# Optimization experiments

Measured on AMD Instinct MI355X. Metric: run time of the kernel, lower is better.

The kernel has to match this reference:

```python
import jax, jax.numpy as jnp
import numpy as np

NB, NL, V, VOCAB, D, TOPK = 16, 64, 16384, 32000, 256, 16
NITER, EARLY, RW = 8, 2, 0.8


def setup_inputs():
    key = jax.random.key(0)
    ks = jax.random.split(key, 8)
    probas = jax.random.uniform(ks[0], (NB, NL, V), dtype=jnp.float32) + 1e-6
    h_d = jax.random.normal(ks[1], (NB, NL, D), dtype=jnp.float32)
    lengths = jax.random.randint(ks[2], (NB,), NL // 2, NL + 1)
    mask = (jnp.arange(NL)[None, :] < lengths[:, None]).astype(jnp.int32)  # prefix mask
    batch_vocab = jax.random.randint(ks[3], (V,), 0, VOCAB)
    emb_table = jax.random.normal(ks[4], (VOCAB, D), dtype=jnp.float32) * 0.02
    W1 = jax.random.normal(ks[5], (2 * D, D), dtype=jnp.float32) * 0.006
    b1 = jnp.zeros((D,), dtype=jnp.float32)
    return {"probas": probas, "h_d": h_d, "mask": mask, "batch_vocab": batch_vocab,
            "emb_table": emb_table, "W1": W1, "b1": b1}


def _forward(probas, h_d, mask, batch_vocab, emb_table, W1, b1):
    maskf = mask.astype(probas.dtype)
    MAP = jnp.argmax(probas, axis=-1)                       # [nb,nl]
    topk_vals, topk_idx = jax.lax.top_k(probas, TOPK)       # [nb,nl,K]
    topk_vals = jnp.where(mask[..., None] < 1, 1.0, topk_vals)
    logits = jnp.log(topk_vals)                             # Categorical(probs) == categorical(log p)
    sLens = jnp.sum(mask, axis=1)                           # [nb]
    one_hot = jnp.arange(NL)[None, :] == (sLens - 1)[:, None]  # one_hot_by_mask: last valid pos
    m2d = (mask[:, :, None] * mask[:, None, :]) > 0
    eyeM = jnp.eye(NL, dtype=probas.dtype)
    h_masked = h_d * maskf[..., None]

    def step(carry, k):
        max_score, best, count, stopped = carry
        choice = jax.random.categorical(k, logits)          # [nb,nl]
        samples = jnp.take_along_axis(topk_idx, choice[..., None], axis=-1)[..., 0]
        samples = jnp.where(one_hot, MAP, samples)
        embs = emb_table[batch_vocab[samples]] * maskf[..., None]   # gather+embed, masked
        new_embs = jax.nn.relu(jnp.concatenate([embs, h_masked], axis=-1) @ W1 + b1)
        Kmat = jnp.einsum('bld,bmd->blm', new_embs, new_embs)       # [nb,nl,nl]
        # det of leading lxl submatrix == det with padded rows/cols replaced by identity
        score = jnp.linalg.det(jnp.where(m2d, Kmat, eyeM))          # [nb]
        improved = score > max_score
        any_imp = jnp.any(improved)
        count = jnp.where(any_imp, 0, count + 1)
        upd = improved & (~stopped)
        stopped = stopped | ((~any_imp) & (count >= EARLY))
        max_score = jnp.where(upd, score, max_score)
        best = jnp.where(upd[:, None], samples, best)
        return (max_score, best, count, stopped), None

    init = (jnp.full((NB,), -jnp.inf, probas.dtype), MAP, jnp.int32(0), jnp.bool_(False))
    keys = jax.random.split(jax.random.key(42), NITER)
    (max_score, best, _, _), _ = jax.lax.scan(step, init, keys)

    # diverse_proba: scatter redist_weight at best choice, (1-rw) elsewhere, renormalize
    am = jnp.where(jnp.arange(V)[None, None, :] == best[:, :, None], RW, 1.0 - RW).astype(probas.dtype)
    x = probas * am
    nm = jnp.sum(x, axis=-1, keepdims=True)
    nm = jnp.where(maskf[..., None] == 0, 1e-10, nm)
    return x / nm, max_score


def reference(probas, h_d, mask, batch_vocab, emb_table, W1, b1):
    return _forward(probas, h_d, mask, batch_vocab, emb_table, W1, b1)
```

## Files before the change

kernel.cpp:

```cpp
#include <hip/hip_runtime.h>
#include <math.h>
#include <stdint.h>


#define TINYF 1.17549435082228750797e-38f

#define KMX(r, c) (((r) * 68) + ((c) ^ ((((r) >> 3) & 7) << 2)))

struct Keys16 { uint32_t k[16]; };

__host__ __device__ inline void tf2x32(uint32_t k0, uint32_t k1,
                                       uint32_t x0, uint32_t x1,
                                       uint32_t* o0, uint32_t* o1) {
  uint32_t ks2 = k0 ^ k1 ^ 0x1BD11BDAu;
  uint32_t ks[3] = {k0, k1, ks2};
  uint32_t v0 = x0 + k0, v1 = x1 + k1;
  const int R0[4] = {13, 15, 26, 6};
  const int R1[4] = {17, 29, 16, 24};
#pragma unroll
  for (int g = 0; g < 5; ++g) {
    const int* RR = (g & 1) ? R1 : R0;
#pragma unroll
    for (int r = 0; r < 4; ++r) {
      v0 += v1;
      v1 = (v1 << RR[r]) | (v1 >> (32 - RR[r]));
      v1 ^= v0;
    }
    v0 += ks[(g + 1) % 3];
    v1 += ks[(g + 2) % 3] + (uint32_t)(g + 1);
  }
  *o0 = v0; *o1 = v1;
}

__device__ inline float logf_ref(float x) { return (float)log((double)x); }

__device__ inline unsigned long long u64max(unsigned long long a,
                                            unsigned long long b) {
  return (a > b) ? a : b;
}

__device__ inline float lane_bcast_f32(float v, int slane) {
  return __uint_as_float(
      (unsigned)__builtin_amdgcn_readlane(__float_as_int(v), slane));
}

template <int CTRL, int RMASK>
__device__ inline void dpp_max_step(unsigned& hi, unsigned& lo) {
  unsigned nh = (unsigned)__builtin_amdgcn_update_dpp(
      0, (int)hi, CTRL, RMASK, 0xF, false);
  unsigned nl = (unsigned)__builtin_amdgcn_update_dpp(
      0, (int)lo, CTRL, RMASK, 0xF, false);
  bool take = (nh > hi) || (nh == hi && nl > lo);
  hi = take ? nh : hi;
  lo = take ? nl : lo;
}

__device__ inline void dpp_reduce_max64(unsigned& hi, unsigned& lo) {
  dpp_max_step<0x111, 0xF>(hi, lo);
  dpp_max_step<0x112, 0xF>(hi, lo);
  dpp_max_step<0x114, 0xF>(hi, lo);
  dpp_max_step<0x118, 0xF>(hi, lo);
  dpp_max_step<0x142, 0xA>(hi, lo);
  dpp_max_step<0x143, 0xC>(hi, lo);
}

__global__ __launch_bounds__(256) void k_topk(const float* __restrict__ probas,
                                              const int* __restrict__ mask,
                                              int* __restrict__ topk_idx,
                                              float* __restrict__ logits,
                                              float* __restrict__ S) {
  int row = blockIdx.x;
  int t = threadIdx.x;
  const float* p = probas + (size_t)row * 16384;
  __shared__ unsigned long long lists[256][16];
  __shared__ float swsum[4];
  __shared__ int lcnt;
  unsigned long long* cand = &lists[0][0];

  cand[t] = 0ull;
  cand[t + 256] = 0ull;
  if (t == 0) lcnt = 0;
  __syncthreads();

  const uint32_t TB = 0x3F7E0000u;
  float sum = 0.f;
  const float4* p4 = (const float4*)p;
#pragma unroll 4
  for (int j = 0; j < 16; ++j) {
    float4 x = p4[t + j * 256];
    int v0 = (t + j * 256) * 4;
    uint32_t u0 = __float_as_uint(x.x), u1 = __float_as_uint(x.y);
    uint32_t u2 = __float_as_uint(x.z), u3 = __float_as_uint(x.w);
    sum += x.x; sum += x.y; sum += x.z; sum += x.w;
    uint32_t um = max(max(u0, u1), max(u2, u3));
    if (um >= TB) {
      if (u0 >= TB) { int s = atomicAdd(&lcnt, 1); if (s < 512)
          cand[s] = ((unsigned long long)u0 << 32) | (unsigned)(~(v0 + 0)); }
      if (u1 >= TB) { int s = atomicAdd(&lcnt, 1); if (s < 512)
          cand[s] = ((unsigned long long)u1 << 32) | (unsigned)(~(v0 + 1)); }
      if (u2 >= TB) { int s = atomicAdd(&lcnt, 1); if (s < 512)
          cand[s] = ((unsigned long long)u2 << 32) | (unsigned)(~(v0 + 2)); }
      if (u3 >= TB) { int s = atomicAdd(&lcnt, 1); if (s < 512)
          cand[s] = ((unsigned long long)u3 << 32) | (unsigned)(~(v0 + 3)); }
    }
  }
#pragma unroll
  for (int off = 32; off >= 1; off >>= 1) sum += __shfl_down(sum, off);
  if ((t & 63) == 0) swsum[t >> 6] = sum;
  __syncthreads();
  if (t == 0) S[row] = ((swsum[0] + swsum[1]) + swsum[2]) + swsum[3];

  int n = lcnt;
  if (n >= 16 && n <= 512) {
    if (t < 64) {
      unsigned long long c[8];
#pragma unroll
      for (int k = 0; k < 8; ++k) c[k] = cand[t + 64 * k];
      unsigned long long win = 0ull;
#pragma unroll
      for (int r = 0; r < 16; ++r) {
        unsigned long long m = c[0];
#pragma unroll
        for (int k = 1; k < 8; ++k) m = u64max(m, c[k]);
#pragma unroll
        for (int off = 32; off >= 1; off >>= 1) {
          unsigned long long o = __shfl_xor(m, off);
          m = u64max(m, o);
        }
        if (t == r) win = m;
#pragma unroll
        for (int k = 0; k < 8; ++k) if (c[k] == m) c[k] = 0ull;
      }
      if (t < 16) {
        int idx = (int)(~(unsigned)(win & 0xFFFFFFFFull));
        float val = __uint_as_float((unsigned)(win >> 32));
        topk_idx[row * 16 + t] = idx;
        logits[row * 16 + t] = (mask[row] == 0) ? 0.0f : logf_ref(val);
      }
    }
    return;
  }

  {
    unsigned long long loc[16];
#pragma unroll
    for (int q = 0; q < 16; ++q) loc[q] = 0ull;
    for (int j = 0; j < 64; ++j) {
      int v = t + j * 256;
      float x = p[v];
      unsigned long long key =
          ((unsigned long long)__float_as_uint(x) << 32) | (unsigned)(~v);
      if (key > loc[15]) {
        loc[15] = key;
#pragma unroll
        for (int q = 15; q > 0; --q) {
          if (loc[q] > loc[q - 1]) {
            unsigned long long tmp = loc[q]; loc[q] = loc[q - 1]; loc[q - 1] = tmp;
          }
        }
      }
    }
    __syncthreads();
#pragma unroll
    for (int q = 0; q < 16; ++q) lists[t][q] = loc[q];
    __syncthreads();
    for (int nl = 128; nl >= 1; nl >>= 1) {
      if (t < nl) {
        unsigned long long M[16];
        int ia = 0, ib = 0;
#pragma unroll
        for (int q = 0; q < 16; ++q) {
          unsigned long long av = lists[t][ia];
          unsigned long long bv = lists[t + nl][ib];
          if (av >= bv) { M[q] = av; ia++; } else { M[q] = bv; ib++; }
        }
#pragma unroll
        for (int q = 0; q < 16; ++q) lists[t][q] = M[q];
      }
      __syncthreads();
    }
    if (t < 16) {
      unsigned long long key = lists[0][t];
      int idx = (int)(~(unsigned)(key & 0xFFFFFFFFull));
      float val = __uint_as_float((unsigned)(key >> 32));
      topk_idx[row * 16 + t] = idx;
      logits[row * 16 + t] = (mask[row] == 0) ? 0.0f : logf_ref(val);
    }
  }
}

__global__ __launch_bounds__(256) void k_sample(Keys16 keys,
                                                const int* __restrict__ mask,
                                                const int* __restrict__ topk_idx,
                                                const float* __restrict__ logits,
                                                int* __restrict__ samples,
                                                int* __restrict__ choice) {
  int tid = blockIdx.x * 256 + threadIdx.x;
  int i = tid >> 10;
  int rbl = tid & 1023;
  int b = rbl >> 6;
  int l = rbl & 63;
  uint32_t k0 = keys.k[2 * i], k1 = keys.k[2 * i + 1];
  int sl = 0;
  for (int m = 0; m < 64; ++m) sl += mask[b * 64 + m];
  float bestv = 0.f; int bestk = 0;
#pragma unroll
  for (int k = 0; k < 16; ++k) {
    uint32_t j = (uint32_t)((b * 64 + l) * 16 + k);
    uint32_t y0, y1;
    tf2x32(k0, k1, 0u, j, &y0, &y1);
    uint32_t bits = y0 ^ y1;
    float f = __uint_as_float((bits >> 9) | 0x3f800000u) - 1.0f;
    float u = fmaxf(TINYF, f * 1.0f + TINYF);
    float t1 = logf_ref(u);
    float g = -logf_ref(-t1);
    float sv = g + logits[rbl * 16 + k];
    if (k == 0 || sv > bestv) { bestv = sv; bestk = k; }
  }
  int ce = (l == sl - 1) ? 0 : bestk;
  choice[tid] = ce;
  samples[tid] = topk_idx[rbl * 16 + ce];
}

__global__ __launch_bounds__(256) void k_ce(const int* __restrict__ topk_idx,
                                            const int* __restrict__ batch_vocab,
                                            const float* __restrict__ emb,
                                            const float* __restrict__ W1,
                                            const float* __restrict__ h_d,
                                            const float* __restrict__ b1,
                                            const int* __restrict__ mask,
                                            const int* __restrict__ choice,
                                            float* __restrict__ Eall) {
  int row = blockIdx.x;
  int t = threadIdx.x;
  __shared__ int smb;
  __shared__ int rid[8];
  __shared__ float e[8][256];
  __shared__ float hl[256];
  if (t == 0) smb = 0;
  float mkf = (float)mask[row];
  hl[t] = h_d[(size_t)row * 256 + t] * mkf;
  __syncthreads();
  if (t < 8) atomicOr(&smb, 1 << choice[t * 1024 + row]);
  __syncthreads();
  int mb = smb;
  if (t < 8) {
    int cnt = __popc(mb);
    int ss = (t < cnt) ? t : 0;
    int kk = 0;
    for (int bit = 0; bit < 16; ++bit) {
      if ((mb >> bit) & 1) {
        if (ss == 0) { kk = bit; break; }
        ss--;
      }
    }
    rid[t] = batch_vocab[topk_idx[row * 16 + kk]];
  }
  __syncthreads();
#pragma unroll
  for (int k = 0; k < 8; ++k) e[k][t] = emb[(size_t)rid[k] * 256 + t];
  __syncthreads();
  float acch = 0.f;
  for (int j0 = 0; j0 < 256; j0 += 4) {
    float4 hv = *(const float4*)&hl[j0];
    float w0 = W1[(256 + j0 + 0) * 256 + t];
    float w1 = W1[(256 + j0 + 1) * 256 + t];
    float w2 = W1[(256 + j0 + 2) * 256 + t];
    float w3 = W1[(256 + j0 + 3) * 256 + t];
    acch = fmaf(hv.x, w0, acch);
    acch = fmaf(hv.y, w1, acch);
    acch = fmaf(hv.z, w2, acch);
    acch = fmaf(hv.w, w3, acch);
  }
  float acc[8];
#pragma unroll
  for (int k = 0; k < 8; ++k) acc[k] = 0.f;
  for (int j0 = 0; j0 < 256; j0 += 4) {
    float w0 = W1[(j0 + 0) * 256 + t];
    float w1 = W1[(j0 + 1) * 256 + t];
    float w2 = W1[(j0 + 2) * 256 + t];
    float w3 = W1[(j0 + 3) * 256 + t];
#pragma unroll
    for (int k = 0; k < 8; ++k) {
      float4 ev = *(const float4*)&e[k][j0];
      acc[k] = fmaf(ev.x, w0, acc[k]);
      acc[k] = fmaf(ev.y, w1, acc[k]);
      acc[k] = fmaf(ev.z, w2, acc[k]);
      acc[k] = fmaf(ev.w, w3, acc[k]);
    }
  }
  float b1v = b1[t];
#pragma unroll
  for (int k = 0; k < 8; ++k) {
    float val = fmaf(mkf, acc[k], acch) + b1v;
    Eall[((size_t)row * 8 + k) * 256 + t] = fmaxf(val, 0.0f);
  }
}

__global__ __launch_bounds__(256, 1) void k_gram(const float* __restrict__ Eall,
                                                 const int* __restrict__ mask,
                                                 const int* __restrict__ choice,
                                                 float* __restrict__ scores) {
  int blk = blockIdx.x;
  int i = blk >> 4, b = blk & 15;
  int t = threadIdx.x;
  __shared__ __align__(16) float Ett[64][68];
  __shared__ __align__(16) float KmF[64 * 68];
  __shared__ int ch[64];
  int mskv = 0;
  if (t < 64) {
    int rowi = b * 64 + t;
    int ml = 0;
#pragma unroll
    for (int ii = 0; ii < 8; ++ii) ml |= 1 << choice[ii * 1024 + rowi];
    int cc = choice[i * 1024 + rowi];
    ch[t] = __popc(ml & ((1 << cc) - 1));
    mskv = mask[rowi];
  }
  __syncthreads();
  int l = t & 63, wd = t >> 6;
  const float* eptr =
      Eall + ((size_t)((b * 64 + l) * 8 + ch[l])) * 256 + wd * 16;
  float acc[16];
#pragma unroll
  for (int q = 0; q < 16; ++q) acc[q] = 0.f;
  int tx = t & 15, ty = t >> 4;
  for (int dt = 0; dt < 4; ++dt) {
    const float* src = eptr + dt * 64;
    float4 v0 = *(const float4*)(src + 0);
    float4 v1 = *(const float4*)(src + 4);
    float4 v2 = *(const float4*)(src + 8);
    float4 v3 = *(const float4*)(src + 12);
    int d0 = wd * 16;
    Ett[d0 +  0][l] = v0.x; Ett[d0 +  1][l] = v0.y;
    Ett[d0 +  2][l] = v0.z; Ett[d0 +  3][l] = v0.w;
    Ett[d0 +  4][l] = v1.x; Ett[d0 +  5][l] = v1.y;
    Ett[d0 +  6][l] = v1.z; Ett[d0 +  7][l] = v1.w;
    Ett[d0 +  8][l] = v2.x; Ett[d0 +  9][l] = v2.y;
    Ett[d0 + 10][l] = v2.z; Ett[d0 + 11][l] = v2.w;
    Ett[d0 + 12][l] = v3.x; Ett[d0 + 13][l] = v3.y;
    Ett[d0 + 14][l] = v3.z; Ett[d0 + 15][l] = v3.w;
    __syncthreads();
#pragma unroll 4
    for (int dd = 0; dd < 64; ++dd) {
      float4 av4 = *(const float4*)&Ett[dd][tx * 4];
      float4 bv4 = *(const float4*)&Ett[dd][ty * 4];
      float avv[4] = {av4.x, av4.y, av4.z, av4.w};
      float bvv[4] = {bv4.x, bv4.y, bv4.z, bv4.w};
#pragma unroll
      for (int a2 = 0; a2 < 4; ++a2)
#pragma unroll
        for (int c2 = 0; c2 < 4; ++c2)
          acc[a2 * 4 + c2] = fmaf(avv[a2], bvv[c2], acc[a2 * 4 + c2]);
    }
    __syncthreads();
  }
#pragma unroll
  for (int a2 = 0; a2 < 4; ++a2)
#pragma unroll
    for (int c2 = 0; c2 < 4; ++c2)
      KmF[KMX(tx * 4 + a2, ty * 4 + c2)] = acc[a2 * 4 + c2];
  __syncthreads();
  if (t >= 64) return;

  unsigned long long bal = __ballot(mskv != 0);
  int L = __popcll(bal);

#define KM_DECL(i) float4 r##i = *(const float4*)&KmF[KMX(t, 4 * i)];
  KM_DECL(0)  KM_DECL(1)  KM_DECL(2)  KM_DECL(3)
  KM_DECL(4)  KM_DECL(5)  KM_DECL(6)  KM_DECL(7)
  KM_DECL(8)  KM_DECL(9)  KM_DECL(10) KM_DECL(11)
  KM_DECL(12) KM_DECL(13) KM_DECL(14) KM_DECL(15)
#undef KM_DECL

  float sdet = 1.f, ssign = 1.f;
  int pos = t;
  float curcol = r0.x;
  float nextcol = r0.y;

  unsigned khi, klo;
  {
    bool cnd = (pos < L);
    khi = cnd ? __float_as_uint(fabsf(curcol)) : 0u;
    klo = cnd ? ((((unsigned)(63 - pos)) << 6) | (unsigned)t) : 0u;
    dpp_reduce_max64(khi, klo);
  }

#pragma unroll 1
  for (int p = 0; p < L; ++p) {
    unsigned lo63 = (unsigned)__builtin_amdgcn_readlane((int)klo, 63);
    int srb = (int)(lo63 & 63u);
    int pb = 63 - (int)((lo63 >> 6) & 63u);
    float kpp = lane_bcast_f32(curcol, srb);
    sdet *= kpp;
    if (pb != p) ssign = -ssign;
    int np = pos;
    if (pos == p) np = pb;
    if (t == srb) np = p;
    pos = np;
    bool active = (pos > p) && (pos < L);
    float f = (active && kpp != 0.f) ? (curcol / kpp) : 0.f;
    float nf = -f;
    float prn = lane_bcast_f32(nextcol, srb);
    float nc1 = fmaf(nf, prn, nextcol);
    int pp1 = p + 1, pp2 = p + 2;
    {
      bool cndn = (pos >= pp1) && (pos < L);
      khi = cndn ? __float_as_uint(fabsf(nc1)) : 0u;
      klo = cndn ? ((((unsigned)(63 - pos)) << 6) | (unsigned)t) : 0u;
      dpp_reduce_max64(khi, klo);
    }
    float cap = nc1;
#define KM_ELIM(i)                                                        \
    if (4 * i + 3 >= pp1) {                                               \
      float px = lane_bcast_f32(r##i.x, srb);                             \
      float py = lane_bcast_f32(r##i.y, srb);                             \
      float pz = lane_bcast_f32(r##i.z, srb);                             \
      float pw = lane_bcast_f32(r##i.w, srb);                             \
      r##i.x = fmaf(nf, px, r##i.x);                                      \
      r##i.y = fmaf(nf, py, r##i.y);                                      \
      r##i.z = fmaf(nf, pz, r##i.z);                                      \
      r##i.w = fmaf(nf, pw, r##i.w);                                      \
      if ((pp2 >> 2) == i) {          \
        int sel = pp2 & 3;                                                \
        cap = (sel == 0) ? r##i.x : (sel == 1) ? r##i.y                   \
            : (sel == 2) ? r##i.z : r##i.w;                               \
      }                                                                   \
    }
    KM_ELIM(0)  KM_ELIM(1)  KM_ELIM(2)  KM_ELIM(3)
    KM_ELIM(4)  KM_ELIM(5)  KM_ELIM(6)  KM_ELIM(7)
    KM_ELIM(8)  KM_ELIM(9)  KM_ELIM(10) KM_ELIM(11)
    KM_ELIM(12) KM_ELIM(13) KM_ELIM(14) KM_ELIM(15)
#undef KM_ELIM
    curcol = nc1;
    nextcol = cap;
  }
  if (t == 0) scores[i * 16 + b] = sdet * ssign;
}

__global__ __launch_bounds__(256) void k_out(const float* __restrict__ probas,
                                             const int* __restrict__ mask,
                                             const int* __restrict__ samples,
                                             const int* __restrict__ topk_idx,
                                             const float* __restrict__ scores,
                                             const float* __restrict__ S,
                                             float* __restrict__ out,
                                             float* __restrict__ out_ms) {
  int row = blockIdx.x;
  int b = row >> 6;
  int t = threadIdx.x;
  __shared__ float ssc[128];
  if (t < 128) ssc[t] = scores[t];
  __syncthreads();
  float ms[16]; int w[16];
#pragma unroll
  for (int q = 0; q < 16; ++q) { ms[q] = -INFINITY; w[q] = -1; }
  int count = 0; bool stopped = false;
#pragma unroll
  for (int i = 0; i < 8; ++i) {
    bool any = false; bool imp[16];
#pragma unroll
    for (int q = 0; q < 16; ++q) {
      imp[q] = ssc[i * 16 + q] > ms[q];
      any = any || imp[q];
    }
    count = any ? 0 : (count + 1);
#pragma unroll
    for (int q = 0; q < 16; ++q) {
      if (imp[q] && !stopped) { ms[q] = ssc[i * 16 + q]; w[q] = i; }
    }
    stopped = stopped || ((!any) && (count >= 2));
  }
  if (row == 0 && t == 0) {
#pragma unroll
    for (int q = 0; q < 16; ++q) out_ms[q] = ms[q];
  }
  int wi = -1;
#pragma unroll
  for (int q = 0; q < 16; ++q) if (b == q) wi = w[q];

  int best = (wi >= 0) ? samples[wi * 1024 + row] : topk_idx[row * 16];
  const float* p = probas + (size_t)row * 16384;
  float* o = out + (size_t)row * 16384;
  float nm;
  if (mask[row] == 0) {
    nm = 1e-10f;
  } else {
    nm = 0.2f * S[row] + 0.6f * p[best];
  }
  const float4* p4 = (const float4*)p;
  float4* o4 = (float4*)o;
  for (int f = t; f < 4096; f += 256) {
    float4 x = p4[f];
    int v0 = f << 2;
    float4 r;
    r.x = x.x * ((v0 + 0 == best) ? 0.8f : 0.2f) / nm;
    r.y = x.y * ((v0 + 1 == best) ? 0.8f : 0.2f) / nm;
    r.z = x.z * ((v0 + 2 == best) ? 0.8f : 0.2f) / nm;
    r.w = x.w * ((v0 + 3 == best) ? 0.8f : 0.2f) / nm;
    o4[f] = r;
  }
}

extern "C" void kernel_launch(void* const* d_in, const int* in_sizes, int n_in,
                              void* d_out, int out_size, void* d_ws, size_t ws_size,
                              hipStream_t stream) {
  const float* probas = (const float*)d_in[0];
  const float* h_d    = (const float*)d_in[1];
  const int*   mask   = (const int*)d_in[2];
  const int*   bvoc   = (const int*)d_in[3];
  const float* emb    = (const float*)d_in[4];
  const float* W1     = (const float*)d_in[5];
  const float* b1     = (const float*)d_in[6];
  float* out = (float*)d_out;

  char* w = (char*)d_ws;
  int*   topk_idx = (int*)w;   w += 16384 * sizeof(int);
  float* logits   = (float*)w; w += 16384 * sizeof(float);
  float* S        = (float*)w; w += 1024 * sizeof(float);
  int*   samples  = (int*)w;   w += 8192 * sizeof(int);
  int*   choice   = (int*)w;   w += 8192 * sizeof(int);
  float* scores   = (float*)w; w += 128 * sizeof(float);

  float* Eall = out;

  Keys16 keys;
  for (uint32_t i = 0; i < 8; ++i) {
    uint32_t a, bq;
    tf2x32(0u, 42u, 0u, i, &a, &bq);
    keys.k[2 * i] = a; keys.k[2 * i + 1] = bq;
  }

  k_topk<<<1024, 256, 0, stream>>>(probas, mask, topk_idx, logits, S);
  k_sample<<<32, 256, 0, stream>>>(keys, mask, topk_idx, logits, samples, choice);
  k_ce<<<1024, 256, 0, stream>>>(topk_idx, bvoc, emb, W1, h_d, b1, mask, choice,
                                 Eall);
  k_gram<<<128, 256, 0, stream>>>(Eall, mask, choice, scores);
  k_out<<<1024, 256, 0, stream>>>(probas, mask, samples, topk_idx, scores, S,
                                  out, out + 16777216);
}
```

Measured before the change: 277.0 us.

## Split determinant elimination columns across four wavefronts with LDS pivot exchange

The LU-based determinant in k_gram previously ran on a single 64-lane wavefront, with each lane holding a full 64-column row in registers. It now spreads the columns over all four wavefronts, 16 columns each. The wavefront that owns the current pivot column finds the pivot and publishes the multipliers and pivot info through double-buffered LDS. Each step now needs a block barrier, which may cost more than the per-wave work it saves.

```diff
diff --git a/kernel.cpp b/kernel.cpp
--- a/kernel.cpp
+++ b/kernel.cpp
@@ -307,7 +307,8 @@
   __shared__ __align__(16) float Ett[64][68];
   __shared__ __align__(16) float KmF[64 * 68];
   __shared__ int ch[64];
-  int mskv = 0;
+  int row = t & 63, cg = t >> 6;
+  int mskv = mask[b * 64 + row];
   if (t < 64) {
     int rowi = b * 64 + t;
     int ml = 0;
@@ -315,10 +316,9 @@
     for (int ii = 0; ii < 8; ++ii) ml |= 1 << choice[ii * 1024 + rowi];
     int cc = choice[i * 1024 + rowi];
     ch[t] = __popc(ml & ((1 << cc) - 1));
-    mskv = mask[rowi];
-  }
-  __syncthreads();
-  int l = t & 63, wd = t >> 6;
+  }
+  __syncthreads();
+  int l = row, wd = cg;
   const float* eptr =
       Eall + ((size_t)((b * 64 + l) * 8 + ch[l])) * 256 + wd * 16;
   float acc[16];
@@ -361,79 +361,84 @@
     for (int c2 = 0; c2 < 4; ++c2)
       KmF[KMX(tx * 4 + a2, ty * 4 + c2)] = acc[a2 * 4 + c2];
   __syncthreads();
-  if (t >= 64) return;
 
   unsigned long long bal = __ballot(mskv != 0);
   int L = __popcll(bal);
 
-#define KM_DECL(i) float4 r##i = *(const float4*)&KmF[KMX(t, 4 * i)];
-  KM_DECL(0)  KM_DECL(1)  KM_DECL(2)  KM_DECL(3)
-  KM_DECL(4)  KM_DECL(5)  KM_DECL(6)  KM_DECL(7)
-  KM_DECL(8)  KM_DECL(9)  KM_DECL(10) KM_DECL(11)
-  KM_DECL(12) KM_DECL(13) KM_DECL(14) KM_DECL(15)
-#undef KM_DECL
-
+  float* fb = &Ett[0][0];
+  unsigned* pinf = (unsigned*)&Ett[2][0];
+
+  float4 c0 = *(const float4*)&KmF[KMX(row, cg * 16 + 0)];
+  float4 c1 = *(const float4*)&KmF[KMX(row, cg * 16 + 4)];
+  float4 c2 = *(const float4*)&KmF[KMX(row, cg * 16 + 8)];
+  float4 c3 = *(const float4*)&KmF[KMX(row, cg * 16 + 12)];
+
+  int pos = row;
   float sdet = 1.f, ssign = 1.f;
-  int pos = t;
-  float curcol = r0.x;
-  float nextcol = r0.y;
-
-  unsigned khi, klo;
-  {
-    bool cnd = (pos < L);
-    khi = cnd ? __float_as_uint(fabsf(curcol)) : 0u;
-    klo = cnd ? ((((unsigned)(63 - pos)) << 6) | (unsigned)t) : 0u;
+  float f_loc = 0.f, kpp_loc = 0.f;
+  int srb_loc = 0, pb_loc = 0;
+
+  auto phaseA = [&](int p) {
+    int li = p - cg * 16;
+    int q = li >> 2, s3 = li & 3;
+    float4 cq;
+    if (q == 0) cq = c0; else if (q == 1) cq = c1;
+    else if (q == 2) cq = c2; else cq = c3;
+    float scol = (s3 == 0) ? cq.x : (s3 == 1) ? cq.y
+               : (s3 == 2) ? cq.z : cq.w;
+    bool cnd = (pos >= p) && (pos < L);
+    unsigned khi = cnd ? __float_as_uint(fabsf(scol)) : 0u;
+    unsigned klo = cnd ? ((((unsigned)(63 - pos)) << 6) | (unsigned)row) : 0u;
     dpp_reduce_max64(khi, klo);
-  }
+    unsigned lo63 = (unsigned)__builtin_amdgcn_readlane((int)klo, 63);
+    int srb = __builtin_amdgcn_readfirstlane((int)(lo63 & 63u));
+    int pb = 63 - (int)((lo63 >> 6) & 63u);
+    float kpp = lane_bcast_f32(scol, srb);
+    int np = pos;
+    if (pos == p) np = pb;
+    if (row == srb) np = p;
+    bool act = (np > p) && (np < L);
+    float f = (act && kpp != 0.f) ? (scol / kpp) : 0.f;
+    int buf = p & 1;
+    fb[buf * 64 + row] = f;
+    if (row == 0) {
+      pinf[buf * 2 + 0] = __float_as_uint(kpp);
+      pinf[buf * 2 + 1] = (unsigned)(srb | (pb << 6));
+    }
+    f_loc = f; kpp_loc = kpp; srb_loc = srb; pb_loc = pb;
+  };
+
+  if (cg == 0) phaseA(0);
 
 #pragma unroll 1
   for (int p = 0; p < L; ++p) {
-    unsigned lo63 = (unsigned)__builtin_amdgcn_readlane((int)klo, 63);
-    int srb = (int)(lo63 & 63u);
-    int pb = 63 - (int)((lo63 >> 6) & 63u);
-    float kpp = lane_bcast_f32(curcol, srb);
+    __syncthreads();
+    int buf = p & 1;
+    bool owner = (cg == (p >> 4));
+    float kpp, f; int srb, pb;
+    if (owner) {
+      kpp = kpp_loc; f = f_loc; srb = srb_loc; pb = pb_loc;
+    } else {
+      kpp = __uint_as_float(pinf[buf * 2 + 0]);
+      unsigned pi = pinf[buf * 2 + 1];
+      srb = __builtin_amdgcn_readfirstlane((int)(pi & 63u));
+      pb = (int)((pi >> 6) & 63u);
+      f = fb[buf * 64 + row];
+    }
     sdet *= kpp;
     if (pb != p) ssign = -ssign;
-    int np = pos;
-    if (pos == p) np = pb;
-    if (t == srb) np = p;
-    pos = np;
-    bool active = (pos > p) && (pos < L);
-    float f = (active && kpp != 0.f) ? (curcol / kpp) : 0.f;
-    float nf = -f;
-    float prn = lane_bcast_f32(nextcol, srb);
-    float nc1 = fmaf(nf, prn, nextcol);
-    int pp1 = p + 1, pp2 = p + 2;
-    {
-      bool cndn = (pos >= pp1) && (pos < L);
-      khi = cndn ? __float_as_uint(fabsf(nc1)) : 0u;
-      klo = cndn ? ((((unsigned)(63 - pos)) << 6) | (unsigned)t) : 0u;
-      dpp_reduce_max64(khi, klo);
-    }
-    float cap = nc1;
-#define KM_ELIM(i)                                                        \
-    if (4 * i + 3 >= pp1) {                                               \
-      float px = lane_bcast_f32(r##i.x, srb);                             \
-      float py = lane_bcast_f32(r##i.y, srb);                             \
-      float pz = lane_bcast_f32(r##i.z, srb);                             \
-      float pw = lane_bcast_f32(r##i.w, srb);                             \
-      r##i.x = fmaf(nf, px, r##i.x);                                      \
-      r##i.y = fmaf(nf, py, r##i.y);                                      \
-      r##i.z = fmaf(nf, pz, r##i.z);                                      \
-      r##i.w = fmaf(nf, pw, r##i.w);                                      \
-      if ((pp2 >> 2) == i) {          \
-        int sel = pp2 & 3;                                                \
-        cap = (sel == 0) ? r##i.x : (sel == 1) ? r##i.y                   \
-            : (sel == 2) ? r##i.z : r##i.w;                               \
-      }                                                                   \
-    }
-    KM_ELIM(0)  KM_ELIM(1)  KM_ELIM(2)  KM_ELIM(3)
-    KM_ELIM(4)  KM_ELIM(5)  KM_ELIM(6)  KM_ELIM(7)
-    KM_ELIM(8)  KM_ELIM(9)  KM_ELIM(10) KM_ELIM(11)
-    KM_ELIM(12) KM_ELIM(13) KM_ELIM(14) KM_ELIM(15)
-#undef KM_ELIM
-    curcol = nc1;
-    nextcol = cap;
+    if (pos == p) pos = pb;
+    if (row == srb) pos = p;
+    if (cg * 16 + 15 >= p + 1) {
+      float nf = -f;
+#define ELIM1(X) X = fmaf(nf, lane_bcast_f32(X, srb), X)
+      ELIM1(c0.x); ELIM1(c0.y); ELIM1(c0.z); ELIM1(c0.w);
+      ELIM1(c1.x); ELIM1(c1.y); ELIM1(c1.z); ELIM1(c1.w);
+      ELIM1(c2.x); ELIM1(c2.y); ELIM1(c2.z); ELIM1(c2.w);
+      ELIM1(c3.x); ELIM1(c3.y); ELIM1(c3.z); ELIM1(c3.w);
+#undef ELIM1
+    }
+    if (p + 1 < L && cg == ((p + 1) >> 4)) phaseA(p + 1);
   }
   if (t == 0) scores[i * 16 + b] = sdet * ssign;
 }
```

New measurement: 351.7 us. 1.27x slower.
